# Kernel tuning notes

Hardware: AMD Instinct MI355X
Metric: run time of the kernel (lower is better)

## Reference

```python
import jax, jax.numpy as jnp
import numpy as np

B, T, D, H = 4, 2048, 1024, 16
HD = D // H  # head_dim = 64

def setup_inputs() -> dict:
    key = jax.random.key(0)
    k1, k2, k3 = jax.random.split(key, 3)
    s = 1.0 / np.sqrt(D)
    return {
        "x": jax.random.normal(k1, (B, T, D), dtype=jnp.float32),
        "w_qkv": jax.random.normal(k2, (D, 3 * D), dtype=jnp.float32) * s,
        "b_qkv": jnp.zeros((3 * D,), dtype=jnp.float32),
        "w_proj": jax.random.normal(k3, (D, D), dtype=jnp.float32) * s,
        "b_proj": jnp.zeros((D,), dtype=jnp.float32),
    }

def reference(x, w_qkv, b_qkv, w_proj, b_proj):
    b, t, c = x.shape
    qkv = x @ w_qkv + b_qkv                       # [B,T,3D]
    qkv = qkv.reshape(b, t, 3, H, HD)
    q, k, v = (jnp.transpose(qkv[:, :, i], (0, 2, 1, 3)) for i in range(3))  # [B,H,T,HD]
    scale = 1.0 / np.sqrt(HD)
    attn = jnp.einsum('bhqd,bhkd->bhqk', q, k) * scale  # [B,H,T,T]
    attn = jax.nn.softmax(attn, axis=-1)
    out = jnp.einsum('bhqk,bhkd->bhqd', attn, v)        # [B,H,T,HD]
    out = jnp.transpose(out, (0, 2, 1, 3)).reshape(b, t, c)
    return out @ w_proj + b_proj
```

## Files before the change

kernel.cpp:

```cpp
#include <hip/hip_runtime.h>
#include <hip/hip_bf16.h>

#define T_SEQ   2048
#define D_MODEL 1024
#define N_HEADS 16
#define HEAD_DIM 64
#define BT      8192
#define N3D     3072

using short8  = __attribute__((ext_vector_type(8))) short;
using short4v = __attribute__((ext_vector_type(4))) short;
using floatx4 = __attribute__((ext_vector_type(4))) float;

#define QSCALE 0.18033688f

__device__ __forceinline__ unsigned short rne_bf16(float f) {
  unsigned int u = __float_as_uint(f);
  u = (u + 0x7fffu + ((u >> 16) & 1u)) >> 16;
  return (unsigned short)u;
}

__device__ __forceinline__ void gload_lds16(const unsigned short* g,
                                            unsigned short* l) {
  __builtin_amdgcn_global_load_lds(
      (const __attribute__((address_space(1))) void*)g,
      (__attribute__((address_space(3))) void*)l, 16, 0, 0);
}

__global__ __launch_bounds__(256) void k_convert(const float* __restrict__ in,
                                                 unsigned short* __restrict__ out) {
  size_t i = ((size_t)blockIdx.x * 256 + threadIdx.x) * 8;
  float4 a = *(const float4*)(in + i);
  float4 b = *(const float4*)(in + i + 4);
  short8 v;
  v[0] = (short)rne_bf16(a.x); v[1] = (short)rne_bf16(a.y);
  v[2] = (short)rne_bf16(a.z); v[3] = (short)rne_bf16(a.w);
  v[4] = (short)rne_bf16(b.x); v[5] = (short)rne_bf16(b.y);
  v[6] = (short)rne_bf16(b.z); v[7] = (short)rne_bf16(b.w);
  *(short8*)(((short*)out) + i) = v;
}

__global__ __launch_bounds__(256) void k_transpose_convert(
    const float* __restrict__ in, unsigned short* __restrict__ out_hi,
    int R, int C) {
  __shared__ float tile[64][65];
  int tiles_c = C >> 6;
  int r0 = (blockIdx.x / tiles_c) << 6;
  int c0 = (blockIdx.x % tiles_c) << 6;
  int tid = threadIdx.x;
#pragma unroll
  for (int i = 0; i < 16; ++i) {
    int idx = tid + i * 256;
    int r = idx >> 6, c = idx & 63;
    tile[r][c] = in[(size_t)(r0 + r) * C + c0 + c];
  }
  __syncthreads();
#pragma unroll
  for (int i = 0; i < 16; ++i) {
    int idx = tid + i * 256;
    int orow = idx >> 6, oc = idx & 63;
    out_hi[(size_t)(c0 + orow) * R + r0 + oc] = rne_bf16(tile[oc][orow]);
  }
}

__global__ __launch_bounds__(256) void k_qkv_gemm(
    const unsigned short* __restrict__ A, const unsigned short* __restrict__ Bt,
    const float* __restrict__ bias,
    unsigned short* __restrict__ Qo, unsigned short* __restrict__ Ko,
    unsigned short* __restrict__ Vt) {
  __shared__ __align__(16) unsigned short As[128 * 32];
  __shared__ __align__(16) unsigned short Bs[128 * 32];
  int tid = threadIdx.x;
  int m0 = (blockIdx.x / 24) * 128;
  int n0 = (blockIdx.x % 24) * 128;
  int w = tid >> 6, lane = tid & 63, quad = lane >> 4, l16 = lane & 15;
  int wm = (w >> 1) * 64, wn = (w & 1) * 64;
  floatx4 acc[4][4] = {};

  int s_row[2], s_sp[2];
#pragma unroll
  for (int i = 0; i < 2; ++i) {
    int u = tid + i * 256;
    s_row[i] = u >> 2;
    s_sp[i] = (u & 3) ^ ((s_row[i] >> 1) & 3);
  }
  int a_off[4], b_off[4];
#pragma unroll
  for (int t = 0; t < 4; ++t) {
    int ra = wm + t * 16 + l16, rb = wn + t * 16 + l16;
    a_off[t] = ra * 32 + (quad ^ ((ra >> 1) & 3)) * 8;
    b_off[t] = rb * 32 + (quad ^ ((rb >> 1) & 3)) * 8;
  }

  for (int k0 = 0; k0 < 1024; k0 += 32) {
#pragma unroll
    for (int i = 0; i < 2; ++i) {
      int ub = (tid & ~63) + i * 256;
      gload_lds16(A + (size_t)(m0 + s_row[i]) * 1024 + k0 + s_sp[i] * 8,
                  &As[ub * 8]);
      gload_lds16(Bt + (size_t)(n0 + s_row[i]) * 1024 + k0 + s_sp[i] * 8,
                  &Bs[ub * 8]);
    }
    __syncthreads();
    short8 af[4], bf[4];
#pragma unroll
    for (int mt = 0; mt < 4; ++mt) af[mt] = *(const short8*)(&As[a_off[mt]]);
#pragma unroll
    for (int nt = 0; nt < 4; ++nt) bf[nt] = *(const short8*)(&Bs[b_off[nt]]);
#pragma unroll
    for (int mt = 0; mt < 4; ++mt)
#pragma unroll
      for (int nt = 0; nt < 4; ++nt)
        acc[mt][nt] = __builtin_amdgcn_mfma_f32_16x16x32_bf16(af[mt], bf[nt],
                                                              acc[mt][nt], 0, 0, 0);
    __syncthreads();
  }

#pragma unroll
  for (int nt = 0; nt < 4; ++nt) {
    int n = n0 + wn + nt * 16 + l16;
    float bv = bias[n];
    int which = n >> 10;
    int nn = n & 1023;
    int h = nn >> 6, hd = nn & 63;
#pragma unroll
    for (int mt = 0; mt < 4; ++mt) {
      int mbase = m0 + wm + mt * 16 + quad * 4;
      int b = mbase >> 11;
      int t0 = mbase & 2047;
      int head = b * N_HEADS + h;
      if (which == 2) {
        short4v vv;
#pragma unroll
        for (int r = 0; r < 4; ++r) vv[r] = (short)rne_bf16(acc[mt][nt][r] + bv);
        *(short4v*)(&Vt[((size_t)head * HEAD_DIM + hd) * T_SEQ + t0]) = vv;
      } else {
        unsigned short* dst = (which == 0) ? Qo : Ko;
        float scl = (which == 0) ? QSCALE : 1.0f;
#pragma unroll
        for (int r = 0; r < 4; ++r)
          dst[((size_t)head * T_SEQ + t0 + r) * HEAD_DIM + hd] =
              rne_bf16((acc[mt][nt][r] + bv) * scl);
      }
    }
  }
}

__global__ __launch_bounds__(256) void k_attn(
    const unsigned short* __restrict__ Q, const unsigned short* __restrict__ K,
    const unsigned short* __restrict__ Vt, unsigned short* __restrict__ Oo) {
  __shared__ __align__(16) unsigned short Klds[64 * 64];
  __shared__ __align__(16) unsigned short Vlds[64 * 64];
  __shared__ __align__(16) unsigned short Plds[4][2][16 * 64];
  int tid = threadIdx.x;
  int head = blockIdx.x >> 4;
  int qb = (blockIdx.x & 15) << 7;
  int b = head >> 4, h = head & 15;
  int w = tid >> 6, lane = tid & 63, quad = lane >> 4, l16 = lane & 15;
  const unsigned short* Qh = Q + (size_t)head * T_SEQ * HEAD_DIM;
  const unsigned short* Kh = K + (size_t)head * T_SEQ * HEAD_DIM;
  const unsigned short* Vh = Vt + (size_t)head * HEAD_DIM * T_SEQ;

  short8 qf[2][2];
#pragma unroll
  for (int qi = 0; qi < 2; ++qi) {
    int qrow = qb + w * 32 + qi * 16 + l16;
#pragma unroll
    for (int ks = 0; ks < 2; ++ks)
      qf[qi][ks] = *(const short8*)(Qh + (size_t)qrow * 64 + ks * 32 + quad * 8);
  }

  short8 ones;
#pragma unroll
  for (int j = 0; j < 8; ++j) ones[j] = (short)0x3F80;

  floatx4 O[2][4] = {};
  floatx4 Osum[2] = {};
  const floatx4 zf = {};

  int sg[2], sidx[2], sub[2];
#pragma unroll
  for (int i = 0; i < 2; ++i) {
    sg[i] = (tid + i * 256) >> 6;
    sidx[i] = lane ^ sg[i];
    sub[i] = (tid & ~63) + i * 256;
  }

  for (int kb = 0; kb < 32; ++kb) {
#pragma unroll
    for (int i = 0; i < 2; ++i) {
      gload_lds16(Kh + ((size_t)(kb * 64 + sidx[i])) * 64 + sg[i] * 8,
                  &Klds[sub[i] * 8]);
      gload_lds16(Vh + (size_t)sidx[i] * T_SEQ + kb * 64 + sg[i] * 8,
                  &Vlds[sub[i] * 8]);
    }
    __syncthreads();

    floatx4 s[2][4];
#pragma unroll
    for (int ks = 0; ks < 2; ++ks) {
      int gk = ks * 4 + quad;
#pragma unroll
      for (int nt = 0; nt < 4; ++nt) {
        int PU = ((gk << 6) + nt * 16 + l16) ^ gk;
        short8 kf = *(const short8*)(&Klds[PU * 8]);
        if (ks == 0) {
          s[0][nt] = __builtin_amdgcn_mfma_f32_16x16x32_bf16(qf[0][0], kf, zf, 0, 0, 0);
          s[1][nt] = __builtin_amdgcn_mfma_f32_16x16x32_bf16(qf[1][0], kf, zf, 0, 0, 0);
        } else {
          s[0][nt] = __builtin_amdgcn_mfma_f32_16x16x32_bf16(qf[0][1], kf, s[0][nt], 0, 0, 0);
          s[1][nt] = __builtin_amdgcn_mfma_f32_16x16x32_bf16(qf[1][1], kf, s[1][nt], 0, 0, 0);
        }
      }
    }

#pragma unroll
    for (int qi = 0; qi < 2; ++qi) {
#pragma unroll
      for (int nt = 0; nt < 4; ++nt) {
        int key = nt * 16 + l16;
        int kg = key >> 3;
        int e = key & 7;
        int U0 = kg * 16 + quad * 4;
        float p0 = __builtin_amdgcn_exp2f(s[qi][nt][0]);
        float p1 = __builtin_amdgcn_exp2f(s[qi][nt][1]);
        float p2 = __builtin_amdgcn_exp2f(s[qi][nt][2]);
        float p3 = __builtin_amdgcn_exp2f(s[qi][nt][3]);
        __hip_bfloat162 lo2 = __float22bfloat162_rn(make_float2(p0, p1));
        __hip_bfloat162 hi2 = __float22bfloat162_rn(make_float2(p2, p3));
        unsigned int blo = *(unsigned int*)&lo2;
        unsigned int bhi = *(unsigned int*)&hi2;
        Plds[w][qi][((U0 + 0) ^ kg) * 8 + e] = (unsigned short)blo;
        Plds[w][qi][((U0 + 1) ^ kg) * 8 + e] = (unsigned short)(blo >> 16);
        Plds[w][qi][((U0 + 2) ^ kg) * 8 + e] = (unsigned short)bhi;
        Plds[w][qi][((U0 + 3) ^ kg) * 8 + e] = (unsigned short)(bhi >> 16);
      }
    }

#pragma unroll
    for (int ks = 0; ks < 2; ++ks) {
      int gk = ks * 4 + quad;
      int PUp = ((gk << 4) + l16) ^ gk;
      short8 pf0 = *(const short8*)(&Plds[w][0][PUp * 8]);
      short8 pf1 = *(const short8*)(&Plds[w][1][PUp * 8]);
      Osum[0] = __builtin_amdgcn_mfma_f32_16x16x32_bf16(pf0, ones, Osum[0], 0, 0, 0);
      Osum[1] = __builtin_amdgcn_mfma_f32_16x16x32_bf16(pf1, ones, Osum[1], 0, 0, 0);
#pragma unroll
      for (int dt = 0; dt < 4; ++dt) {
        int PUv = ((gk << 6) + dt * 16 + l16) ^ gk;
        short8 vf = *(const short8*)(&Vlds[PUv * 8]);
        O[0][dt] = __builtin_amdgcn_mfma_f32_16x16x32_bf16(pf0, vf, O[0][dt], 0, 0, 0);
        O[1][dt] = __builtin_amdgcn_mfma_f32_16x16x32_bf16(pf1, vf, O[1][dt], 0, 0, 0);
      }
    }
    __syncthreads();
  }

#pragma unroll
  for (int qi = 0; qi < 2; ++qi) {
    float inv[4];
#pragma unroll
    for (int r = 0; r < 4; ++r) inv[r] = 1.0f / Osum[qi][r];
#pragma unroll
    for (int dt = 0; dt < 4; ++dt)
#pragma unroll
      for (int r = 0; r < 4; ++r) {
        float val = O[qi][dt][r] * inv[r];
        int t = qb + w * 32 + qi * 16 + quad * 4 + r;
        size_t o = ((size_t)(b * T_SEQ + t)) * D_MODEL + h * HEAD_DIM + dt * 16 + l16;
        Oo[o] = rne_bf16(val);
      }
  }
}

__global__ __launch_bounds__(256) void k_proj_gemm(
    const unsigned short* __restrict__ A, const unsigned short* __restrict__ Bt,
    const float* __restrict__ bias, float* __restrict__ out) {
  __shared__ __align__(16) unsigned short As[128 * 32];
  __shared__ __align__(16) unsigned short Bs[128 * 32];
  int tid = threadIdx.x;
  int m0 = (blockIdx.x >> 3) * 128;
  int n0 = (blockIdx.x & 7) * 128;
  int w = tid >> 6, lane = tid & 63, quad = lane >> 4, l16 = lane & 15;
  int wm = (w >> 1) * 64, wn = (w & 1) * 64;
  floatx4 acc[4][4] = {};

  int s_row[2], s_sp[2];
#pragma unroll
  for (int i = 0; i < 2; ++i) {
    int u = tid + i * 256;
    s_row[i] = u >> 2;
    s_sp[i] = (u & 3) ^ ((s_row[i] >> 1) & 3);
  }
  int a_off[4], b_off[4];
#pragma unroll
  for (int t = 0; t < 4; ++t) {
    int ra = wm + t * 16 + l16, rb = wn + t * 16 + l16;
    a_off[t] = ra * 32 + (quad ^ ((ra >> 1) & 3)) * 8;
    b_off[t] = rb * 32 + (quad ^ ((rb >> 1) & 3)) * 8;
  }

  for (int k0 = 0; k0 < 1024; k0 += 32) {
#pragma unroll
    for (int i = 0; i < 2; ++i) {
      int ub = (tid & ~63) + i * 256;
      gload_lds16(A + (size_t)(m0 + s_row[i]) * 1024 + k0 + s_sp[i] * 8,
                  &As[ub * 8]);
      gload_lds16(Bt + (size_t)(n0 + s_row[i]) * 1024 + k0 + s_sp[i] * 8,
                  &Bs[ub * 8]);
    }
    __syncthreads();
    short8 af[4], bf[4];
#pragma unroll
    for (int mt = 0; mt < 4; ++mt) af[mt] = *(const short8*)(&As[a_off[mt]]);
#pragma unroll
    for (int nt = 0; nt < 4; ++nt) bf[nt] = *(const short8*)(&Bs[b_off[nt]]);
#pragma unroll
    for (int mt = 0; mt < 4; ++mt)
#pragma unroll
      for (int nt = 0; nt < 4; ++nt)
        acc[mt][nt] = __builtin_amdgcn_mfma_f32_16x16x32_bf16(af[mt], bf[nt],
                                                              acc[mt][nt], 0, 0, 0);
    __syncthreads();
  }

#pragma unroll
  for (int nt = 0; nt < 4; ++nt) {
    int n = n0 + wn + nt * 16 + l16;
    float bv = bias[n];
#pragma unroll
    for (int mt = 0; mt < 4; ++mt)
#pragma unroll
      for (int r = 0; r < 4; ++r) {
        int m = m0 + wm + mt * 16 + quad * 4 + r;
        out[(size_t)m * 1024 + n] = acc[mt][nt][r] + bv;
      }
  }
}

extern "C" void kernel_launch(void* const* d_in, const int* in_sizes, int n_in,
                              void* d_out, int out_size, void* d_ws, size_t ws_size,
                              hipStream_t stream) {
  const float* x     = (const float*)d_in[0];
  const float* wqkv  = (const float*)d_in[1];
  const float* bqkv  = (const float*)d_in[2];
  const float* wproj = (const float*)d_in[3];
  const float* bproj = (const float*)d_in[4];

  char* ws = (char*)d_ws;
  size_t off = 0;
  unsigned short* x_bf  = (unsigned short*)(ws + off); off += (size_t)BT * D_MODEL * 2;
  unsigned short* wq_T  = (unsigned short*)(ws + off); off += (size_t)N3D * D_MODEL * 2;
  unsigned short* wp_T  = (unsigned short*)(ws + off); off += (size_t)D_MODEL * D_MODEL * 2;
  unsigned short* Qb    = (unsigned short*)(ws + off); off += (size_t)BT * D_MODEL * 2;
  unsigned short* Kb    = (unsigned short*)(ws + off); off += (size_t)BT * D_MODEL * 2;
  unsigned short* Vt    = (unsigned short*)(ws + off); off += (size_t)BT * D_MODEL * 2;
  unsigned short* a_bf  = (unsigned short*)(ws + off); off += (size_t)BT * D_MODEL * 2;

  k_convert<<<(BT * D_MODEL) / (256 * 8), 256, 0, stream>>>(x, x_bf);
  k_transpose_convert<<<(1024 / 64) * (3072 / 64), 256, 0, stream>>>(wqkv, wq_T, 1024, 3072);
  k_transpose_convert<<<(1024 / 64) * (1024 / 64), 256, 0, stream>>>(wproj, wp_T, 1024, 1024);
  k_qkv_gemm<<<(BT / 128) * (N3D / 128), 256, 0, stream>>>(x_bf, wq_T, bqkv, Qb, Kb, Vt);
  k_attn<<<(T_SEQ / 128) * 4 * N_HEADS, 256, 0, stream>>>(Qb, Kb, Vt, a_bf);
  k_proj_gemm<<<(BT / 128) * (D_MODEL / 128), 256, 0, stream>>>(a_bf, wp_T, bproj, (float*)d_out);
}
```

Before: 333.8 us.

## Keep softmax probabilities in registers by transposing attention MFMAs

The S and PV MFMAs now use swapped operands, computing transposed tiles so that each lane's exp'd probabilities already sit in the B-operand layout for the PV product. This removes the per-wave P staging buffer in LDS, with its scalar 16-bit stores and reloads. K rows are loaded into LDS in a permuted order so the score columns line up with the register layout. The output write becomes a vectorised 4-element bf16 store per row, and the row sum is taken from a single accumulator element.

```diff
diff --git a/kernel.cpp b/kernel.cpp
--- a/kernel.cpp
+++ b/kernel.cpp
@@ -151,7 +151,6 @@
     const unsigned short* __restrict__ Vt, unsigned short* __restrict__ Oo) {
   __shared__ __align__(16) unsigned short Klds[64 * 64];
   __shared__ __align__(16) unsigned short Vlds[64 * 64];
-  __shared__ __align__(16) unsigned short Plds[4][2][16 * 64];
   int tid = threadIdx.x;
   int head = blockIdx.x >> 4;
   int qb = (blockIdx.x & 15) << 7;
@@ -178,20 +177,23 @@
   floatx4 Osum[2] = {};
   const floatx4 zf = {};
 
-  int sg[2], sidx[2], sub[2];
+  int sg[2], sub[2], ksrc[2], vsrc[2];
 #pragma unroll
   for (int i = 0; i < 2; ++i) {
     sg[i] = (tid + i * 256) >> 6;
-    sidx[i] = lane ^ sg[i];
     sub[i] = (tid & ~63) + i * 256;
+    int xs = lane ^ sg[i];
+    int ntp = xs >> 4, mp = xs & 15;
+    ksrc[i] = ((ntp >> 1) << 5) + ((mp >> 2) << 3) + ((ntp & 1) << 2) + (mp & 3);
+    vsrc[i] = xs;
   }
 
   for (int kb = 0; kb < 32; ++kb) {
 #pragma unroll
     for (int i = 0; i < 2; ++i) {
-      gload_lds16(Kh + ((size_t)(kb * 64 + sidx[i])) * 64 + sg[i] * 8,
+      gload_lds16(Kh + ((size_t)(kb * 64 + ksrc[i])) * 64 + sg[i] * 8,
                   &Klds[sub[i] * 8]);
-      gload_lds16(Vh + (size_t)sidx[i] * T_SEQ + kb * 64 + sg[i] * 8,
+      gload_lds16(Vh + (size_t)vsrc[i] * T_SEQ + kb * 64 + sg[i] * 8,
                   &Vlds[sub[i] * 8]);
     }
     __syncthreads();
@@ -205,52 +207,52 @@
         int PU = ((gk << 6) + nt * 16 + l16) ^ gk;
         short8 kf = *(const short8*)(&Klds[PU * 8]);
         if (ks == 0) {
-          s[0][nt] = __builtin_amdgcn_mfma_f32_16x16x32_bf16(qf[0][0], kf, zf, 0, 0, 0);
-          s[1][nt] = __builtin_amdgcn_mfma_f32_16x16x32_bf16(qf[1][0], kf, zf, 0, 0, 0);
+          s[0][nt] = __builtin_amdgcn_mfma_f32_16x16x32_bf16(kf, qf[0][0], zf, 0, 0, 0);
+          s[1][nt] = __builtin_amdgcn_mfma_f32_16x16x32_bf16(kf, qf[1][0], zf, 0, 0, 0);
         } else {
-          s[0][nt] = __builtin_amdgcn_mfma_f32_16x16x32_bf16(qf[0][1], kf, s[0][nt], 0, 0, 0);
-          s[1][nt] = __builtin_amdgcn_mfma_f32_16x16x32_bf16(qf[1][1], kf, s[1][nt], 0, 0, 0);
+          s[0][nt] = __builtin_amdgcn_mfma_f32_16x16x32_bf16(kf, qf[0][1], s[0][nt], 0, 0, 0);
+          s[1][nt] = __builtin_amdgcn_mfma_f32_16x16x32_bf16(kf, qf[1][1], s[1][nt], 0, 0, 0);
         }
       }
     }
 
+    short8 pB[2][2];
 #pragma unroll
     for (int qi = 0; qi < 2; ++qi) {
+      unsigned int dw[4][2];
 #pragma unroll
       for (int nt = 0; nt < 4; ++nt) {
-        int key = nt * 16 + l16;
-        int kg = key >> 3;
-        int e = key & 7;
-        int U0 = kg * 16 + quad * 4;
         float p0 = __builtin_amdgcn_exp2f(s[qi][nt][0]);
         float p1 = __builtin_amdgcn_exp2f(s[qi][nt][1]);
         float p2 = __builtin_amdgcn_exp2f(s[qi][nt][2]);
         float p3 = __builtin_amdgcn_exp2f(s[qi][nt][3]);
         __hip_bfloat162 lo2 = __float22bfloat162_rn(make_float2(p0, p1));
         __hip_bfloat162 hi2 = __float22bfloat162_rn(make_float2(p2, p3));
-        unsigned int blo = *(unsigned int*)&lo2;
-        unsigned int bhi = *(unsigned int*)&hi2;
-        Plds[w][qi][((U0 + 0) ^ kg) * 8 + e] = (unsigned short)blo;
-        Plds[w][qi][((U0 + 1) ^ kg) * 8 + e] = (unsigned short)(blo >> 16);
-        Plds[w][qi][((U0 + 2) ^ kg) * 8 + e] = (unsigned short)bhi;
-        Plds[w][qi][((U0 + 3) ^ kg) * 8 + e] = (unsigned short)(bhi >> 16);
+        dw[nt][0] = *(unsigned int*)&lo2;
+        dw[nt][1] = *(unsigned int*)&hi2;
+      }
+#pragma unroll
+      for (int ks = 0; ks < 2; ++ks) {
+        union { unsigned int u[4]; short8 s8; } cv;
+        cv.u[0] = dw[2 * ks][0];
+        cv.u[1] = dw[2 * ks][1];
+        cv.u[2] = dw[2 * ks + 1][0];
+        cv.u[3] = dw[2 * ks + 1][1];
+        pB[qi][ks] = cv.s8;
       }
     }
 
 #pragma unroll
     for (int ks = 0; ks < 2; ++ks) {
       int gk = ks * 4 + quad;
-      int PUp = ((gk << 4) + l16) ^ gk;
-      short8 pf0 = *(const short8*)(&Plds[w][0][PUp * 8]);
-      short8 pf1 = *(const short8*)(&Plds[w][1][PUp * 8]);
-      Osum[0] = __builtin_amdgcn_mfma_f32_16x16x32_bf16(pf0, ones, Osum[0], 0, 0, 0);
-      Osum[1] = __builtin_amdgcn_mfma_f32_16x16x32_bf16(pf1, ones, Osum[1], 0, 0, 0);
+      Osum[0] = __builtin_amdgcn_mfma_f32_16x16x32_bf16(ones, pB[0][ks], Osum[0], 0, 0, 0);
+      Osum[1] = __builtin_amdgcn_mfma_f32_16x16x32_bf16(ones, pB[1][ks], Osum[1], 0, 0, 0);
 #pragma unroll
       for (int dt = 0; dt < 4; ++dt) {
         int PUv = ((gk << 6) + dt * 16 + l16) ^ gk;
         short8 vf = *(const short8*)(&Vlds[PUv * 8]);
-        O[0][dt] = __builtin_amdgcn_mfma_f32_16x16x32_bf16(pf0, vf, O[0][dt], 0, 0, 0);
-        O[1][dt] = __builtin_amdgcn_mfma_f32_16x16x32_bf16(pf1, vf, O[1][dt], 0, 0, 0);
+        O[0][dt] = __builtin_amdgcn_mfma_f32_16x16x32_bf16(vf, pB[0][ks], O[0][dt], 0, 0, 0);
+        O[1][dt] = __builtin_amdgcn_mfma_f32_16x16x32_bf16(vf, pB[1][ks], O[1][dt], 0, 0, 0);
       }
     }
     __syncthreads();
@@ -258,18 +260,16 @@
 
 #pragma unroll
   for (int qi = 0; qi < 2; ++qi) {
-    float inv[4];
-#pragma unroll
-    for (int r = 0; r < 4; ++r) inv[r] = 1.0f / Osum[qi][r];
-#pragma unroll
-    for (int dt = 0; dt < 4; ++dt)
-#pragma unroll
-      for (int r = 0; r < 4; ++r) {
-        float val = O[qi][dt][r] * inv[r];
-        int t = qb + w * 32 + qi * 16 + quad * 4 + r;
-        size_t o = ((size_t)(b * T_SEQ + t)) * D_MODEL + h * HEAD_DIM + dt * 16 + l16;
-        Oo[o] = rne_bf16(val);
-      }
+    float inv = 1.0f / Osum[qi][0];
+    int t = qb + w * 32 + qi * 16 + l16;
+    size_t rowo = ((size_t)(b * T_SEQ + t)) * D_MODEL + h * HEAD_DIM;
+#pragma unroll
+    for (int dt = 0; dt < 4; ++dt) {
+      short4v ov;
+#pragma unroll
+      for (int r = 0; r < 4; ++r) ov[r] = (short)rne_bf16(O[qi][dt][r] * inv);
+      *(short4v*)(&Oo[rowo + dt * 16 + quad * 4]) = ov;
+    }
   }
 }
 
```

Measured after the change: 325.4 us. -2.5%, faster.
